# Performance work log

Hardware: AMD Instinct MI355X
Metric: run time of the kernel (lower is better)

## Reference

```python
import jax, jax.numpy as jnp
import numpy as np

IN_FEATURES = 256
HIDDEN_SIZE = 512
OUT_FEATURES = 256


def setup_inputs() -> dict:
    key = jax.random.key(0)
    k_x, k_w1, k_b1, k_w2, k_b2 = jax.random.split(key, 5)
    batch, seq_len = 64, 2048
    # PyTorch nn.Linear init scale ~ 1/sqrt(fan_in)
    s1 = 1.0 / np.sqrt(IN_FEATURES + HIDDEN_SIZE)
    s2 = 1.0 / np.sqrt(HIDDEN_SIZE)
    return {
        "x": jax.random.normal(k_x, (batch, seq_len, IN_FEATURES), dtype=jnp.float32),
        # W1: [hidden+in, hidden]; concat order in original is (hidden, input)
        "W1": jax.random.uniform(k_w1, (HIDDEN_SIZE + IN_FEATURES, HIDDEN_SIZE), minval=-s1, maxval=s1, dtype=jnp.float32),
        "b1": jax.random.uniform(k_b1, (HIDDEN_SIZE,), minval=-s1, maxval=s1, dtype=jnp.float32),
        "W2": jax.random.uniform(k_w2, (HIDDEN_SIZE, OUT_FEATURES), minval=-s2, maxval=s2, dtype=jnp.float32),
        "b2": jax.random.uniform(k_b2, (OUT_FEATURES,), minval=-s2, maxval=s2, dtype=jnp.float32),
    }


def reference(x, W1, b1, W2, b2):
    # x: [batch, seq, in] -> scan over seq
    batch = x.shape[0]
    # Split W1 into the hidden-part and input-part (concat order: hidden first)
    W1_h = W1[:HIDDEN_SIZE]   # [hidden, hidden]
    W1_x = W1[HIDDEN_SIZE:]   # [in, hidden]
    h0 = jnp.zeros((batch, HIDDEN_SIZE), dtype=x.dtype)

    def step(h, x_t):
        # equivalent to concat([h, x_t], -1) @ W1 + b1
        h_new = jnp.tanh(h @ W1_h + x_t @ W1_x + b1)
        y_t = h_new @ W2 + b2
        return h_new, y_t

    xs = jnp.swapaxes(x, 0, 1)              # [seq, batch, in]
    h_last, ys = jax.lax.scan(step, h0, xs)  # ys: [seq, batch, out]
    output = jnp.swapaxes(ys, 0, 1)          # [batch, seq, out]
    # original returns curr_hidden_state with leading dim 1
    return output, h_last[None, :, :]
```

## Files before the change

kernel.cpp:

```cpp
#include <hip/hip_runtime.h>
#include <math.h>


#define BB 64
#define TT 2048
#define II 256
#define HH 512
#define OO 256
#define NBLK 256
#define OUT_OFF ((size_t)BB * TT * OO)
#define FLAGS_INTS ((TT + 1) * NBLK)

typedef unsigned long long ull;
typedef float fx4 __attribute__((ext_vector_type(4)));

__global__ void rnn_init(int* __restrict__ flags) {
    int i = blockIdx.x * blockDim.x + threadIdx.x;
    if (i < FLAGS_INTS) flags[i] = 0;
}

__global__ __launch_bounds__(256, 1) void rnn_persist(
    const float* __restrict__ x, const float* __restrict__ W1,
    const float* __restrict__ b1, const float* __restrict__ W2,
    const float* __restrict__ b2, float* __restrict__ out,
    int* __restrict__ flags, float* __restrict__ hbuf)
{
    __shared__ float v_s[16 * HH];
    __shared__ float sc_h[128 * 64];
    __shared__ float sc_y[64 * 64];

    const int tid = threadIdx.x;
    const int blk = blockIdx.x;
    const int bi  = blk >> 6;
    const int cj  = blk & 63;
    const int R0  = bi << 4;
    const int C0  = cj << 3;
    const int O0  = cj << 2;

    const int g  = tid & 63;
    const int rq = tid >> 6;

    float w1r[3][4][8];
    #pragma unroll
    for (int jj = 0; jj < 2; ++jj)
        #pragma unroll
        for (int i = 0; i < 4; ++i) {
            const float* wp = W1 + (size_t)((jj << 8) + (g << 2) + i) * HH + C0;
            float4 a = *(const float4*)wp;
            float4 b = *(const float4*)(wp + 4);
            w1r[jj][i][0]=a.x; w1r[jj][i][1]=a.y; w1r[jj][i][2]=a.z; w1r[jj][i][3]=a.w;
            w1r[jj][i][4]=b.x; w1r[jj][i][5]=b.y; w1r[jj][i][6]=b.z; w1r[jj][i][7]=b.w;
        }
    #pragma unroll
    for (int i = 0; i < 4; ++i) {
        const float* wp = W1 + (size_t)(HH + (g << 2) + i) * HH + C0;
        float4 a = *(const float4*)wp;
        float4 b = *(const float4*)(wp + 4);
        w1r[2][i][0]=a.x; w1r[2][i][1]=a.y; w1r[2][i][2]=a.z; w1r[2][i][3]=a.w;
        w1r[2][i][4]=b.x; w1r[2][i][5]=b.y; w1r[2][i][6]=b.z; w1r[2][i][7]=b.w;
    }
    float w2r[2][4][4];
    #pragma unroll
    for (int jj = 0; jj < 2; ++jj)
        #pragma unroll
        for (int i = 0; i < 4; ++i) {
            float4 a = *(const float4*)(W2 + (size_t)((jj << 8) + (g << 2) + i) * OO + O0);
            w2r[jj][i][0]=a.x; w2r[jj][i][1]=a.y; w2r[jj][i][2]=a.z; w2r[jj][i][3]=a.w;
        }
    const float b1v = (tid < 128) ? b1[C0 + (tid & 7)] : 0.f;
    const float b2v = (tid >= 128 && tid < 192) ? b2[O0 + ((tid - 128) & 3)] : 0.f;

    float* hb[2] = { hbuf, hbuf + (size_t)BB * HH };

    #pragma unroll
    for (int m = 0; m < 8; ++m)
        *(float4*)&v_s[((m << 8) + tid) << 2] = make_float4(0.f, 0.f, 0.f, 0.f);

    fx4 xreg[4];
    #pragma unroll
    for (int r = 0; r < 4; ++r)
        xreg[r] = __builtin_nontemporal_load(
            (const fx4*)&x[((size_t)(R0 + rq + (r << 2)) * TT + 0) * II + (g << 2)]);
    __syncthreads();

    for (int t = 0; t < TT; ++t) {
        float pa[4][8];
        float py[4][4];
        #pragma unroll
        for (int r = 0; r < 4; ++r) {
            #pragma unroll
            for (int c = 0; c < 8; ++c) pa[r][c] = 0.f;
            #pragma unroll
            for (int o = 0; o < 4; ++o) py[r][o] = 0.f;
        }
        #pragma unroll
        for (int r = 0; r < 4; ++r) {
            fx4 vv = xreg[r];
            #pragma unroll
            for (int i = 0; i < 4; ++i) {
                const float vi = vv[i];
                #pragma unroll
                for (int c = 0; c < 8; ++c)
                    pa[r][c] = fmaf(vi, w1r[2][i][c], pa[r][c]);
            }
        }
        if (t > 0) {
            const int* fp = flags + (size_t)t * NBLK + (bi << 6) + (tid >> 2);
            while (__hip_atomic_load((int*)fp, __ATOMIC_RELAXED,
                                     __HIP_MEMORY_SCOPE_AGENT) == 0) {}
            const ull* hsrc = (const ull*)hb[t & 1];
            ull* vd = (ull*)v_s;
            #pragma unroll
            for (int half = 0; half < 2; ++half) {
                ull hl[8];
                #pragma unroll
                for (int m = 0; m < 8; ++m) {
                    int row = (half << 3) + m;
                    hl[m] = __hip_atomic_load(
                        (ull*)&hsrc[(size_t)(R0 + row) * (HH / 2) + tid],
                        __ATOMIC_RELAXED, __HIP_MEMORY_SCOPE_AGENT);
                }
                #pragma unroll
                for (int m = 0; m < 8; ++m) {
                    int row = (half << 3) + m;
                    vd[row * (HH / 2) + tid] = hl[m];
                }
            }
        }
        __syncthreads();

        #pragma unroll
        for (int r = 0; r < 4; ++r) {
            const float* vrow = v_s + (rq + (r << 2)) * HH;
            #pragma unroll
            for (int jj = 0; jj < 2; ++jj) {
                float4 vv = *(const float4*)(vrow + (jj << 8) + (g << 2));
                float vva[4] = { vv.x, vv.y, vv.z, vv.w };
                #pragma unroll
                for (int i = 0; i < 4; ++i) {
                    const float vi = vva[i];
                    #pragma unroll
                    for (int c = 0; c < 8; ++c)
                        pa[r][c] = fmaf(vi, w1r[jj][i][c], pa[r][c]);
                    #pragma unroll
                    for (int o = 0; o < 4; ++o)
                        py[r][o] = fmaf(vi, w2r[jj][i][o], py[r][o]);
                }
            }
        }
        #pragma unroll
        for (int r = 0; r < 4; ++r) {
            const int row = rq + (r << 2);
            #pragma unroll
            for (int c = 0; c < 8; ++c) {
                const int u = (row << 3) + c;
                sc_h[(u << 6) + (g ^ ((u & 15) << 2))] = pa[r][c];
            }
            #pragma unroll
            for (int o = 0; o < 4; ++o) {
                const int u = (row << 2) + o;
                sc_y[(u << 6) + (g ^ ((u & 15) << 2))] = py[r][o];
            }
        }
        __syncthreads();

        if (tid < 128) {
            float s = 0.f;
            #pragma unroll
            for (int j = 0; j < 16; ++j) {
                float4 q = *(const float4*)&sc_h[(tid << 6) + ((j << 2) ^ ((tid & 15) << 2))];
                s += (q.x + q.y) + (q.z + q.w);
            }
            float hv = tanhf(s + b1v);
            __hip_atomic_store(&hb[(t + 1) & 1][(size_t)(R0 + (tid >> 3)) * HH + C0 + (tid & 7)],
                               hv, __ATOMIC_RELAXED, __HIP_MEMORY_SCOPE_AGENT);
            if (t == TT - 1)
                out[OUT_OFF + (size_t)(R0 + (tid >> 3)) * HH + C0 + (tid & 7)] = hv;
        } else if (tid < 192 && t > 0) {
            const int u = tid - 128;
            float s = 0.f;
            #pragma unroll
            for (int j = 0; j < 16; ++j) {
                float4 q = *(const float4*)&sc_y[(u << 6) + ((j << 2) ^ ((u & 15) << 2))];
                s += (q.x + q.y) + (q.z + q.w);
            }
            __builtin_nontemporal_store(s + b2v,
                &out[((size_t)(R0 + (u >> 2)) * TT + (t - 1)) * OO + O0 + (u & 3)]);
        }
        asm volatile("s_waitcnt vmcnt(0)" ::: "memory");
        __syncthreads();
        if (tid == 0)
            __hip_atomic_store(&flags[(size_t)(t + 1) * NBLK + blk], 1,
                               __ATOMIC_RELAXED, __HIP_MEMORY_SCOPE_AGENT);
        if (t + 1 < TT) {
            #pragma unroll
            for (int r = 0; r < 4; ++r)
                xreg[r] = __builtin_nontemporal_load(
                    (const fx4*)&x[((size_t)(R0 + rq + (r << 2)) * TT + (t + 1)) * II + (g << 2)]);
        }
    }

    {
        const int* fp = flags + (size_t)TT * NBLK + (bi << 6) + (tid >> 2);
        while (__hip_atomic_load((int*)fp, __ATOMIC_RELAXED,
                                 __HIP_MEMORY_SCOPE_AGENT) == 0) {}
        const ull* hsrc = (const ull*)hb[TT & 1];
        ull* vd = (ull*)v_s;
        #pragma unroll
        for (int half = 0; half < 2; ++half) {
            ull hl[8];
            #pragma unroll
            for (int m = 0; m < 8; ++m) {
                int row = (half << 3) + m;
                hl[m] = __hip_atomic_load(
                    (ull*)&hsrc[(size_t)(R0 + row) * (HH / 2) + tid],
                    __ATOMIC_RELAXED, __HIP_MEMORY_SCOPE_AGENT);
            }
            #pragma unroll
            for (int m = 0; m < 8; ++m) {
                int row = (half << 3) + m;
                vd[row * (HH / 2) + tid] = hl[m];
            }
        }
        __syncthreads();
        float py[4][4];
        #pragma unroll
        for (int r = 0; r < 4; ++r) {
            #pragma unroll
            for (int o = 0; o < 4; ++o) py[r][o] = 0.f;
            const float* vrow = v_s + (rq + (r << 2)) * HH;
            #pragma unroll
            for (int jj = 0; jj < 2; ++jj) {
                float4 vv = *(const float4*)(vrow + (jj << 8) + (g << 2));
                float vva[4] = { vv.x, vv.y, vv.z, vv.w };
                #pragma unroll
                for (int i = 0; i < 4; ++i) {
                    const float vi = vva[i];
                    #pragma unroll
                    for (int o = 0; o < 4; ++o)
                        py[r][o] = fmaf(vi, w2r[jj][i][o], py[r][o]);
                }
            }
            const int row = rq + (r << 2);
            #pragma unroll
            for (int o = 0; o < 4; ++o) {
                const int u = (row << 2) + o;
                sc_y[(u << 6) + (g ^ ((u & 15) << 2))] = py[r][o];
            }
        }
        __syncthreads();
        if (tid >= 128 && tid < 192) {
            const int u = tid - 128;
            float s = 0.f;
            #pragma unroll
            for (int j = 0; j < 16; ++j) {
                float4 q = *(const float4*)&sc_y[(u << 6) + ((j << 2) ^ ((u & 15) << 2))];
                s += (q.x + q.y) + (q.z + q.w);
            }
            out[((size_t)(R0 + (u >> 2)) * TT + (TT - 1)) * OO + O0 + (u & 3)] = s + b2v;
        }
    }
}

extern "C" void kernel_launch(void* const* d_in, const int* in_sizes, int n_in,
                              void* d_out, int out_size, void* d_ws, size_t ws_size,
                              hipStream_t stream) {
    const float* x  = (const float*)d_in[0];
    const float* W1 = (const float*)d_in[1];
    const float* b1 = (const float*)d_in[2];
    const float* W2 = (const float*)d_in[3];
    const float* b2 = (const float*)d_in[4];
    float* out = (float*)d_out;

    float* hbuf  = (float*)d_ws;
    int*   flags = (int*)((char*)d_ws + 512 * 1024);

    rnn_init<<<dim3((FLAGS_INTS + 255) / 256), dim3(256), 0, stream>>>(flags);
    rnn_persist<<<dim3(NBLK), dim3(256), 0, stream>>>(x, W1, b1, W2, b2, out,
                                                      flags, hbuf);
}
```

Baseline: 11.67 ms.

## Precompute input projection with a separate GEMM before the persistent recurrence

Adds a tiled fp32 GEMM that computes x @ W1_x for all timesteps up front into a workspace buffer. The persistent recurrent kernel then reads one precomputed value per output element and skips the per-step input matmul, which shortens the serial critical path and frees registers. The cost is a 256 MB intermediate write and read, plus a fallback to the old kernel when the workspace is too small.

```diff
diff --git a/kernel.cpp b/kernel.cpp
--- a/kernel.cpp
+++ b/kernel.cpp
@@ -10,6 +10,8 @@
 #define NBLK 256
 #define OUT_OFF ((size_t)BB * TT * OO)
 #define FLAGS_INTS ((TT + 1) * NBLK)
+#define XW_OFF (4ull * 1024 * 1024)
+#define XW_BYTES ((size_t)BB * TT * HH * 4)
 
 typedef unsigned long long ull;
 typedef float fx4 __attribute__((ext_vector_type(4)));
@@ -19,7 +21,273 @@
     if (i < FLAGS_INTS) flags[i] = 0;
 }
 
-__global__ __launch_bounds__(256, 1) void rnn_persist(
+__global__ __launch_bounds__(256) void xw_gemm(
+    const float* __restrict__ x, const float* __restrict__ W1,
+    float* __restrict__ xw)
+{
+    __shared__ float As[64][68];
+    __shared__ float Bs[64][68];
+    const int tid = threadIdx.x;
+    const int m0 = (int)(blockIdx.x >> 3) << 6;
+    const int n0 = (int)(blockIdx.x & 7) << 6;
+    const int tx = tid & 15, ty = tid >> 4;
+
+    float acc[4][4];
+    #pragma unroll
+    for (int r = 0; r < 4; ++r)
+        #pragma unroll
+        for (int c = 0; c < 4; ++c) acc[r][c] = 0.f;
+
+    for (int kp = 0; kp < II; kp += 64) {
+        #pragma unroll
+        for (int u = 0; u < 4; ++u) {
+            int e = (u << 8) + tid;
+            int row = e >> 4;
+            int k4  = (e & 15) << 2;
+            float4 v = *(const float4*)&x[(size_t)(m0 + row) * II + kp + k4];
+            As[k4 + 0][row] = v.x; As[k4 + 1][row] = v.y;
+            As[k4 + 2][row] = v.z; As[k4 + 3][row] = v.w;
+            *(float4*)&Bs[row][k4] = *(const float4*)&W1[(size_t)(HH + kp + row) * HH + n0 + k4];
+        }
+        __syncthreads();
+        #pragma unroll 8
+        for (int kk = 0; kk < 64; ++kk) {
+            float4 av = *(const float4*)&As[kk][ty << 2];
+            float4 bv = *(const float4*)&Bs[kk][tx << 2];
+            float aa[4] = { av.x, av.y, av.z, av.w };
+            float bb[4] = { bv.x, bv.y, bv.z, bv.w };
+            #pragma unroll
+            for (int r = 0; r < 4; ++r)
+                #pragma unroll
+                for (int c = 0; c < 4; ++c)
+                    acc[r][c] = fmaf(aa[r], bb[c], acc[r][c]);
+        }
+        __syncthreads();
+    }
+    #pragma unroll
+    for (int r = 0; r < 4; ++r) {
+        float4 v = make_float4(acc[r][0], acc[r][1], acc[r][2], acc[r][3]);
+        *(float4*)&xw[(size_t)(m0 + (ty << 2) + r) * HH + n0 + (tx << 2)] = v;
+    }
+}
+
+__global__ __launch_bounds__(256, 1) void rnn_persist_xw(
+    const float* __restrict__ xwp, const float* __restrict__ W1,
+    const float* __restrict__ b1, const float* __restrict__ W2,
+    const float* __restrict__ b2, float* __restrict__ out,
+    int* __restrict__ flags, float* __restrict__ hbuf)
+{
+    __shared__ float v_s[16 * HH];
+    __shared__ float sc_h[128 * 64];
+    __shared__ float sc_y[64 * 64];
+
+    const int tid = threadIdx.x;
+    const int blk = blockIdx.x;
+    const int bi  = blk >> 6;
+    const int cj  = blk & 63;
+    const int R0  = bi << 4;
+    const int C0  = cj << 3;
+    const int O0  = cj << 2;
+
+    const int g  = tid & 63;
+    const int rq = tid >> 6;
+
+    float w1r[2][4][8];
+    #pragma unroll
+    for (int jj = 0; jj < 2; ++jj)
+        #pragma unroll
+        for (int i = 0; i < 4; ++i) {
+            const float* wp = W1 + (size_t)((jj << 8) + (g << 2) + i) * HH + C0;
+            float4 a = *(const float4*)wp;
+            float4 b = *(const float4*)(wp + 4);
+            w1r[jj][i][0]=a.x; w1r[jj][i][1]=a.y; w1r[jj][i][2]=a.z; w1r[jj][i][3]=a.w;
+            w1r[jj][i][4]=b.x; w1r[jj][i][5]=b.y; w1r[jj][i][6]=b.z; w1r[jj][i][7]=b.w;
+        }
+    float w2r[2][4][4];
+    #pragma unroll
+    for (int jj = 0; jj < 2; ++jj)
+        #pragma unroll
+        for (int i = 0; i < 4; ++i) {
+            float4 a = *(const float4*)(W2 + (size_t)((jj << 8) + (g << 2) + i) * OO + O0);
+            w2r[jj][i][0]=a.x; w2r[jj][i][1]=a.y; w2r[jj][i][2]=a.z; w2r[jj][i][3]=a.w;
+        }
+    const float b1v = (tid < 128) ? b1[C0 + (tid & 7)] : 0.f;
+    const float b2v = (tid >= 128 && tid < 192) ? b2[O0 + ((tid - 128) & 3)] : 0.f;
+
+    float* hb[2] = { hbuf, hbuf + (size_t)BB * HH };
+
+    #pragma unroll
+    for (int m = 0; m < 8; ++m)
+        *(float4*)&v_s[((m << 8) + tid) << 2] = make_float4(0.f, 0.f, 0.f, 0.f);
+    __syncthreads();
+
+    for (int t = 0; t < TT; ++t) {
+        float xwv = 0.f;
+        if (tid < 128)
+            xwv = xwp[((size_t)(R0 + (tid >> 3)) * TT + t) * HH + C0 + (tid & 7)];
+
+        if (t > 0) {
+            const int* fp = flags + (size_t)t * NBLK + (bi << 6) + (tid >> 2);
+            while (__hip_atomic_load((int*)fp, __ATOMIC_RELAXED,
+                                     __HIP_MEMORY_SCOPE_AGENT) == 0) {}
+            const ull* hsrc = (const ull*)hb[t & 1];
+            ull* vd = (ull*)v_s;
+            #pragma unroll
+            for (int half = 0; half < 2; ++half) {
+                ull hl[8];
+                #pragma unroll
+                for (int m = 0; m < 8; ++m) {
+                    int row = (half << 3) + m;
+                    hl[m] = __hip_atomic_load(
+                        (ull*)&hsrc[(size_t)(R0 + row) * (HH / 2) + tid],
+                        __ATOMIC_RELAXED, __HIP_MEMORY_SCOPE_AGENT);
+                }
+                #pragma unroll
+                for (int m = 0; m < 8; ++m) {
+                    int row = (half << 3) + m;
+                    vd[row * (HH / 2) + tid] = hl[m];
+                }
+            }
+        }
+        __syncthreads();
+
+        float pa[4][8];
+        float py[4][4];
+        #pragma unroll
+        for (int r = 0; r < 4; ++r) {
+            #pragma unroll
+            for (int c = 0; c < 8; ++c) pa[r][c] = 0.f;
+            #pragma unroll
+            for (int o = 0; o < 4; ++o) py[r][o] = 0.f;
+        }
+        #pragma unroll
+        for (int r = 0; r < 4; ++r) {
+            const float* vrow = v_s + (rq + (r << 2)) * HH;
+            #pragma unroll
+            for (int jj = 0; jj < 2; ++jj) {
+                float4 vv = *(const float4*)(vrow + (jj << 8) + (g << 2));
+                float vva[4] = { vv.x, vv.y, vv.z, vv.w };
+                #pragma unroll
+                for (int i = 0; i < 4; ++i) {
+                    const float vi = vva[i];
+                    #pragma unroll
+                    for (int c = 0; c < 8; ++c)
+                        pa[r][c] = fmaf(vi, w1r[jj][i][c], pa[r][c]);
+                    #pragma unroll
+                    for (int o = 0; o < 4; ++o)
+                        py[r][o] = fmaf(vi, w2r[jj][i][o], py[r][o]);
+                }
+            }
+        }
+        #pragma unroll
+        for (int r = 0; r < 4; ++r) {
+            const int row = rq + (r << 2);
+            #pragma unroll
+            for (int c = 0; c < 8; ++c) {
+                const int u = (row << 3) + c;
+                sc_h[(u << 6) + (g ^ ((u & 15) << 2))] = pa[r][c];
+            }
+            #pragma unroll
+            for (int o = 0; o < 4; ++o) {
+                const int u = (row << 2) + o;
+                sc_y[(u << 6) + (g ^ ((u & 15) << 2))] = py[r][o];
+            }
+        }
+        __syncthreads();
+
+        if (tid < 128) {
+            float s = 0.f;
+            #pragma unroll
+            for (int j = 0; j < 16; ++j) {
+                float4 q = *(const float4*)&sc_h[(tid << 6) + ((j << 2) ^ ((tid & 15) << 2))];
+                s += (q.x + q.y) + (q.z + q.w);
+            }
+            float hv = tanhf(s + xwv + b1v);
+            __hip_atomic_store(&hb[(t + 1) & 1][(size_t)(R0 + (tid >> 3)) * HH + C0 + (tid & 7)],
+                               hv, __ATOMIC_RELAXED, __HIP_MEMORY_SCOPE_AGENT);
+            if (t == TT - 1)
+                out[OUT_OFF + (size_t)(R0 + (tid >> 3)) * HH + C0 + (tid & 7)] = hv;
+        } else if (tid < 192 && t > 0) {
+            const int u = tid - 128;
+            float s = 0.f;
+            #pragma unroll
+            for (int j = 0; j < 16; ++j) {
+                float4 q = *(const float4*)&sc_y[(u << 6) + ((j << 2) ^ ((u & 15) << 2))];
+                s += (q.x + q.y) + (q.z + q.w);
+            }
+            __builtin_nontemporal_store(s + b2v,
+                &out[((size_t)(R0 + (u >> 2)) * TT + (t - 1)) * OO + O0 + (u & 3)]);
+        }
+        asm volatile("s_waitcnt vmcnt(0)" ::: "memory");
+        __syncthreads();
+        if (tid == 0)
+            __hip_atomic_store(&flags[(size_t)(t + 1) * NBLK + blk], 1,
+                               __ATOMIC_RELAXED, __HIP_MEMORY_SCOPE_AGENT);
+    }
+
+    {
+        const int* fp = flags + (size_t)TT * NBLK + (bi << 6) + (tid >> 2);
+        while (__hip_atomic_load((int*)fp, __ATOMIC_RELAXED,
+                                 __HIP_MEMORY_SCOPE_AGENT) == 0) {}
+        const ull* hsrc = (const ull*)hb[TT & 1];
+        ull* vd = (ull*)v_s;
+        #pragma unroll
+        for (int half = 0; half < 2; ++half) {
+            ull hl[8];
+            #pragma unroll
+            for (int m = 0; m < 8; ++m) {
+                int row = (half << 3) + m;
+                hl[m] = __hip_atomic_load(
+                    (ull*)&hsrc[(size_t)(R0 + row) * (HH / 2) + tid],
+                    __ATOMIC_RELAXED, __HIP_MEMORY_SCOPE_AGENT);
+            }
+            #pragma unroll
+            for (int m = 0; m < 8; ++m) {
+                int row = (half << 3) + m;
+                vd[row * (HH / 2) + tid] = hl[m];
+            }
+        }
+        __syncthreads();
+        float py[4][4];
+        #pragma unroll
+        for (int r = 0; r < 4; ++r) {
+            #pragma unroll
+            for (int o = 0; o < 4; ++o) py[r][o] = 0.f;
+            const float* vrow = v_s + (rq + (r << 2)) * HH;
+            #pragma unroll
+            for (int jj = 0; jj < 2; ++jj) {
+                float4 vv = *(const float4*)(vrow + (jj << 8) + (g << 2));
+                float vva[4] = { vv.x, vv.y, vv.z, vv.w };
+                #pragma unroll
+                for (int i = 0; i < 4; ++i) {
+                    const float vi = vva[i];
+                    #pragma unroll
+                    for (int o = 0; o < 4; ++o)
+                        py[r][o] = fmaf(vi, w2r[jj][i][o], py[r][o]);
+                }
+            }
+            const int row = rq + (r << 2);
+            #pragma unroll
+            for (int o = 0; o < 4; ++o) {
+                const int u = (row << 2) + o;
+                sc_y[(u << 6) + (g ^ ((u & 15) << 2))] = py[r][o];
+            }
+        }
+        __syncthreads();
+        if (tid >= 128 && tid < 192) {
+            const int u = tid - 128;
+            float s = 0.f;
+            #pragma unroll
+            for (int j = 0; j < 16; ++j) {
+                float4 q = *(const float4*)&sc_y[(u << 6) + ((j << 2) ^ ((u & 15) << 2))];
+                s += (q.x + q.y) + (q.z + q.w);
+            }
+            out[((size_t)(R0 + (u >> 2)) * TT + (TT - 1)) * OO + O0 + (u & 3)] = s + b2v;
+        }
+    }
+}
+
+__global__ __launch_bounds__(256, 1) void rnn_persist_fb(
     const float* __restrict__ x, const float* __restrict__ W1,
     const float* __restrict__ b1, const float* __restrict__ W2,
     const float* __restrict__ b2, float* __restrict__ out,
@@ -42,7 +310,7 @@
 
     float w1r[3][4][8];
     #pragma unroll
-    for (int jj = 0; jj < 2; ++jj)
+    for (int jj = 0; jj < 3; ++jj)
         #pragma unroll
         for (int i = 0; i < 4; ++i) {
             const float* wp = W1 + (size_t)((jj << 8) + (g << 2) + i) * HH + C0;
@@ -51,14 +319,6 @@
             w1r[jj][i][0]=a.x; w1r[jj][i][1]=a.y; w1r[jj][i][2]=a.z; w1r[jj][i][3]=a.w;
             w1r[jj][i][4]=b.x; w1r[jj][i][5]=b.y; w1r[jj][i][6]=b.z; w1r[jj][i][7]=b.w;
         }
-    #pragma unroll
-    for (int i = 0; i < 4; ++i) {
-        const float* wp = W1 + (size_t)(HH + (g << 2) + i) * HH + C0;
-        float4 a = *(const float4*)wp;
-        float4 b = *(const float4*)(wp + 4);
-        w1r[2][i][0]=a.x; w1r[2][i][1]=a.y; w1r[2][i][2]=a.z; w1r[2][i][3]=a.w;
-        w1r[2][i][4]=b.x; w1r[2][i][5]=b.y; w1r[2][i][6]=b.z; w1r[2][i][7]=b.w;
-    }
     float w2r[2][4][4];
     #pragma unroll
     for (int jj = 0; jj < 2; ++jj)
@@ -276,6 +536,14 @@
     int*   flags = (int*)((char*)d_ws + 512 * 1024);
 
     rnn_init<<<dim3((FLAGS_INTS + 255) / 256), dim3(256), 0, stream>>>(flags);
-    rnn_persist<<<dim3(NBLK), dim3(256), 0, stream>>>(x, W1, b1, W2, b2, out,
-                                                      flags, hbuf);
+
+    if (ws_size >= XW_OFF + XW_BYTES) {
+        float* xwbuf = (float*)((char*)d_ws + XW_OFF);
+        xw_gemm<<<dim3(16384), dim3(256), 0, stream>>>(x, W1, xwbuf);
+        rnn_persist_xw<<<dim3(NBLK), dim3(256), 0, stream>>>(xwbuf, W1, b1, W2, b2,
+                                                             out, flags, hbuf);
+    } else {
+        rnn_persist_fb<<<dim3(NBLK), dim3(256), 0, stream>>>(x, W1, b1, W2, b2,
+                                                             out, flags, hbuf);
+    }
 }
```

Result: slower. 12.92 ms (+10.8%).
